# Optimization experiments

Hardware: AMD Instinct MI355X
Metric: run time of the kernel (lower is better)

Reference implementation:

```python
import jax, jax.numpy as jnp
import numpy as np

B = 64          # batches
T = 65536       # total packed tokens
X = 512         # token feature dim
K = 5           # io pairs
Y = X * K       # extra dim = 2560
H = 512         # hidden


def setup_inputs() -> dict:
    key = jax.random.key(0)
    ks = jax.random.split(key, 13)
    s = 0.02  # weight scale
    return {
        "ps_data": jax.random.normal(ks[0], (T, X), jnp.float32),
        "io_embed": jax.random.normal(ks[1], (B, K, X), jnp.float32),
        "segment_ids": jnp.sort(jax.random.randint(ks[2], (T,), 0, B, dtype=jnp.int32)),
        # attention_fc: Linear(X+Y,512) -> ReLU -> Linear(512,512) -> ReLU -> Linear(512,1)
        "W1": jax.random.normal(ks[3], (X + Y, H), jnp.float32) * s,
        "b1": jnp.zeros((H,), jnp.float32),
        "W2": jax.random.normal(ks[4], (H, H), jnp.float32) * s,
        "b2": jnp.zeros((H,), jnp.float32),
        "W3": jax.random.normal(ks[5], (H, 1), jnp.float32) * s,
        "b3": jnp.zeros((1,), jnp.float32),
        # final_fc: Linear(512,512) -> ReLU -> Linear(512,2)
        "Wf1": jax.random.normal(ks[6], (H, H), jnp.float32) * s,
        "bf1": jnp.zeros((H,), jnp.float32),
        "Wf2": jax.random.normal(ks[7], (H, 2), jnp.float32) * s,
        "bf2": jnp.zeros((2,), jnp.float32),
    }


def reference(ps_data, io_embed, segment_ids, W1, b1, W2, b2, W3, b3, Wf1, bf1, Wf2, bf2):
    # io_embed (B,K,X) -> (B,Y); gather per token by its batch index
    extra = io_embed.reshape(B, -1)[segment_ids]            # (T, Y)
    h = jnp.concatenate([ps_data, extra], axis=1)           # (T, X+Y)
    h = jax.nn.relu(h @ W1 + b1)
    h = jax.nn.relu(h @ W2 + b2)
    logits = (h @ W3 + b3)[:, 0]                            # (T,)
    # per-segment softmax over ragged segments
    m = jax.lax.stop_gradient(
        jax.ops.segment_max(logits, segment_ids, num_segments=B))
    e = jnp.exp(logits - m[segment_ids])
    denom = jax.ops.segment_sum(e, segment_ids, num_segments=B)
    w = e / denom[segment_ids]                              # (T,)
    pooled = jax.ops.segment_sum(w[:, None] * ps_data, segment_ids,
                                 num_segments=B)            # (B, X)
    # final_fc
    return jax.nn.relu(pooled @ Wf1 + bf1) @ Wf2 + bf2      # (B, 2)
```

## Files before the change

### kernel.cpp

```cpp
#include <hip/hip_runtime.h>

#define T_TOK 65536
#define BATCH 64
#define XDIM  512
#define HDIM  512
#define YDIM  2560

#define BK 64
#define GM_TM 256
#define GM_TN 128

#define SB_KC 64
#define SB_KS 40
#define SB_BG 8

#define PREP_CONV   16384
#define PREP_TRANS  2048
#define PREP_SB     320

typedef float  f32x16 __attribute__((ext_vector_type(16)));
typedef __bf16 bf16x8 __attribute__((ext_vector_type(8)));

__device__ __forceinline__ unsigned short f2bf(float f) {
    unsigned int u = __float_as_uint(f);
    return (unsigned short)((u + 0x7FFFu + ((u >> 16) & 1u)) >> 16);
}

__device__ __forceinline__ float bf2f(unsigned short u) {
    return __uint_as_float((unsigned int)u << 16);
}

__device__ __forceinline__ void load_lds16(const unsigned short* g, unsigned short* l) {
    __builtin_amdgcn_global_load_lds(
        (const __attribute__((address_space(1))) unsigned int*)g,
        (__attribute__((address_space(3))) unsigned int*)l, 16, 0, 0);
}

__device__ __forceinline__ int lower_bound_seg(const int* __restrict__ s, int n, int v) {
    int lo = 0, hi = n;
    while (lo < hi) { int mid = (lo + hi) >> 1; if (s[mid] < v) lo = mid + 1; else hi = mid; }
    return lo;
}

__global__ __launch_bounds__(256) void prep_kernel(const float* __restrict__ ps,
                                                   unsigned short* __restrict__ psb,
                                                   const float* __restrict__ W1,
                                                   const float* __restrict__ W2,
                                                   unsigned short* __restrict__ w1t,
                                                   unsigned short* __restrict__ w2t,
                                                   const float* __restrict__ io,
                                                   float* __restrict__ partial) {
    __shared__ float sio[SB_BG][SB_KC];
    const int blk = blockIdx.x;
    const int t = threadIdx.x;

    if (blk < PREP_CONV) {
        size_t idx = (size_t)blk * 256 + t;
        const float4* s4 = reinterpret_cast<const float4*>(ps) + idx * 2;
        float4 a = s4[0], b = s4[1];
        ushort4 o0, o1;
        o0.x = f2bf(a.x); o0.y = f2bf(a.y); o0.z = f2bf(a.z); o0.w = f2bf(a.w);
        o1.x = f2bf(b.x); o1.y = f2bf(b.y); o1.z = f2bf(b.z); o1.w = f2bf(b.w);
        reinterpret_cast<ushort4*>(psb)[idx * 2 + 0] = o0;
        reinterpret_cast<ushort4*>(psb)[idx * 2 + 1] = o1;
    } else if (blk < PREP_CONV + PREP_TRANS) {
        int bb = blk - PREP_CONV;
        const float* src = bb < 1024 ? W1 : W2;
        unsigned short* dst = bb < 1024 ? w1t : w2t;
        int idx = (bb & 1023) * 256 + t;
        int nn = idx >> 9, kk = idx & 511;
        dst[idx] = f2bf(src[(size_t)kk * 512 + nn]);
    } else {
        int sb = blk - PREP_CONV - PREP_TRANS;
        int s = sb >> 3, g = sb & 7;
        for (int i = t; i < SB_BG * SB_KC; i += 256) {
            int bb = i >> 6, kk = i & 63;
            sio[bb][kk] = io[(size_t)(g * SB_BG + bb) * YDIM + s * SB_KC + kk];
        }
        __syncthreads();
        float acc[SB_BG][2] = {};
        const int k0 = 512 + s * SB_KC;
        #pragma unroll 4
        for (int kk = 0; kk < SB_KC; kk++) {
            float wa = W1[(size_t)(k0 + kk) * 512 + t];
            float wb = W1[(size_t)(k0 + kk) * 512 + t + 256];
            #pragma unroll
            for (int bb = 0; bb < SB_BG; bb++) {
                acc[bb][0] += sio[bb][kk] * wa;
                acc[bb][1] += sio[bb][kk] * wb;
            }
        }
        #pragma unroll
        for (int bb = 0; bb < SB_BG; bb++) {
            int b = g * SB_BG + bb;
            partial[((size_t)s * BATCH + b) * 512 + t]       = acc[bb][0];
            partial[((size_t)s * BATCH + b) * 512 + t + 256] = acc[bb][1];
        }
    }
}

__global__ __launch_bounds__(256) void segbias_reduce(const float* __restrict__ partial,
                                                      float* __restrict__ segbias) {
    int idx = blockIdx.x * 256 + threadIdx.x;
    float s = 0.f;
    #pragma unroll
    for (int i = 0; i < SB_KS; i++) s += partial[(size_t)i * BATCH * 512 + idx];
    segbias[idx] = s;
}

#define FRAG_AT(sh, R, c) (*reinterpret_cast<const bf16x8*>(&(sh)[((R) * 8 + (((c) ^ ((R) & 7)))) * 8]))

__global__ __launch_bounds__(512) void gemm1_kernel(const unsigned short* __restrict__ psb,
                                                    const unsigned short* __restrict__ w1t,
                                                    const float* __restrict__ segbias,
                                                    const float* __restrict__ b1,
                                                    const int* __restrict__ segids,
                                                    unsigned short* __restrict__ h1) {
    __shared__ unsigned short shA[GM_TM * BK];
    __shared__ unsigned short shB[GM_TN * BK];

    const int bid = blockIdx.x;
    const int xcd = bid & 7;
    const int j = bid >> 3;
    const int n0 = (j & 3) * GM_TN;
    const int m0 = ((j >> 2) * 8 + xcd) * GM_TM;
    const int t = threadIdx.x;
    const int w = t >> 6, L = t & 63;
    const int mbase = (w >> 1) * 64, nbase = (w & 1) * 64;
    const int l31 = L & 31, lh = L >> 5;

    f32x16 acc[2][2] = {};

    for (int kt = 0; kt < XDIM; kt += BK) {
        #pragma unroll
        for (int i_ = 0; i_ < 4; i_++) {
            int g_ = i_ * 512 + t;
            int r_ = g_ >> 3, c_ = g_ & 7, cs_ = c_ ^ (r_ & 7);
            load_lds16(psb + (size_t)(m0 + r_) * XDIM + kt + cs_ * 8, &shA[g_ * 8]);
        }
        #pragma unroll
        for (int i_ = 0; i_ < 2; i_++) {
            int g_ = i_ * 512 + t;
            int r_ = g_ >> 3, c_ = g_ & 7, cs_ = c_ ^ (r_ & 7);
            load_lds16(w1t + (size_t)(n0 + r_) * HDIM + kt + cs_ * 8, &shB[g_ * 8]);
        }
        __syncthreads();
        #pragma unroll
        for (int ks = 0; ks < 4; ks++) {
            const int c = ks * 2 + lh;
            bf16x8 af[2], bfr[2];
            #pragma unroll
            for (int i = 0; i < 2; i++)  af[i]  = FRAG_AT(shA, mbase + i * 32 + l31, c);
            #pragma unroll
            for (int jj = 0; jj < 2; jj++) bfr[jj] = FRAG_AT(shB, nbase + jj * 32 + l31, c);
            #pragma unroll
            for (int i = 0; i < 2; i++)
                #pragma unroll
                for (int jj = 0; jj < 2; jj++)
                    acc[i][jj] = __builtin_amdgcn_mfma_f32_32x32x16_bf16(af[i], bfr[jj], acc[i][jj], 0, 0, 0);
        }
        __syncthreads();
    }

    float b1v[2];
    #pragma unroll
    for (int jj = 0; jj < 2; jj++) b1v[jj] = b1[n0 + nbase + jj * 32 + l31];
    #pragma unroll
    for (int i = 0; i < 2; i++) {
        #pragma unroll
        for (int r = 0; r < 16; r++) {
            int gm = m0 + mbase + i * 32 + (r & 3) + 8 * (r >> 2) + 4 * lh;
            int sg = segids[gm];
            const float* sb = segbias + (size_t)sg * HDIM;
            #pragma unroll
            for (int jj = 0; jj < 2; jj++) {
                int gn = n0 + nbase + jj * 32 + l31;
                float v = acc[i][jj][r] + sb[gn] + b1v[jj];
                v = v > 0.f ? v : 0.f;
                h1[(size_t)gm * HDIM + gn] = f2bf(v);
            }
        }
    }
}

__global__ __launch_bounds__(512) void gemm2_kernel(const unsigned short* __restrict__ h1,
                                                    const unsigned short* __restrict__ w2t,
                                                    const float* __restrict__ b2,
                                                    const float* __restrict__ w3,
                                                    float* __restrict__ logits8) {
    __shared__ unsigned short shA[GM_TM * BK];
    __shared__ unsigned short shB[GM_TN * BK];

    const int bid = blockIdx.x;
    const int xcd = bid & 7;
    const int j = bid >> 3;
    const int n0 = (j & 3) * GM_TN;
    const int m0 = ((j >> 2) * 8 + xcd) * GM_TM;
    const int t = threadIdx.x;
    const int w = t >> 6, L = t & 63;
    const int mbase = (w >> 1) * 64, nbase = (w & 1) * 64;
    const int l31 = L & 31, lh = L >> 5;

    f32x16 acc[2][2] = {};

    for (int kt = 0; kt < HDIM; kt += BK) {
        #pragma unroll
        for (int i_ = 0; i_ < 4; i_++) {
            int g_ = i_ * 512 + t;
            int r_ = g_ >> 3, c_ = g_ & 7, cs_ = c_ ^ (r_ & 7);
            load_lds16(h1 + (size_t)(m0 + r_) * HDIM + kt + cs_ * 8, &shA[g_ * 8]);
        }
        #pragma unroll
        for (int i_ = 0; i_ < 2; i_++) {
            int g_ = i_ * 512 + t;
            int r_ = g_ >> 3, c_ = g_ & 7, cs_ = c_ ^ (r_ & 7);
            load_lds16(w2t + (size_t)(n0 + r_) * HDIM + kt + cs_ * 8, &shB[g_ * 8]);
        }
        __syncthreads();
        #pragma unroll
        for (int ks = 0; ks < 4; ks++) {
            const int c = ks * 2 + lh;
            bf16x8 af[2], bfr[2];
            #pragma unroll
            for (int i = 0; i < 2; i++)  af[i]  = FRAG_AT(shA, mbase + i * 32 + l31, c);
            #pragma unroll
            for (int jj = 0; jj < 2; jj++) bfr[jj] = FRAG_AT(shB, nbase + jj * 32 + l31, c);
            #pragma unroll
            for (int i = 0; i < 2; i++)
                #pragma unroll
                for (int jj = 0; jj < 2; jj++)
                    acc[i][jj] = __builtin_amdgcn_mfma_f32_32x32x16_bf16(af[i], bfr[jj], acc[i][jj], 0, 0, 0);
        }
        __syncthreads();
    }

    float w3v[2], b2v[2];
    #pragma unroll
    for (int jj = 0; jj < 2; jj++) {
        int gn = n0 + nbase + jj * 32 + l31;
        w3v[jj] = w3[gn];
        b2v[jj] = b2[gn];
    }
    const int slice = (j & 3) * 2 + (w & 1);
    #pragma unroll
    for (int i = 0; i < 2; i++) {
        #pragma unroll
        for (int r = 0; r < 16; r++) {
            float p = 0.f;
            #pragma unroll
            for (int jj = 0; jj < 2; jj++) {
                float h2 = acc[i][jj][r] + b2v[jj];
                h2 = h2 > 0.f ? h2 : 0.f;
                p += h2 * w3v[jj];
            }
            p += __shfl_xor(p, 1, 64);
            p += __shfl_xor(p, 2, 64);
            p += __shfl_xor(p, 4, 64);
            p += __shfl_xor(p, 8, 64);
            p += __shfl_xor(p, 16, 64);
            if (l31 == 0)
                logits8[(size_t)slice * T_TOK + m0 + mbase + i * 32 +
                        (r & 3) + 8 * (r >> 2) + 4 * lh] = p;
        }
    }
}

__global__ __launch_bounds__(512) void pool_kernel(const unsigned short* __restrict__ psb,
                                                   const float* __restrict__ logits8,
                                                   const int* __restrict__ segids,
                                                   float* __restrict__ pooled16) {
    const int s = blockIdx.x;
    const int b = blockIdx.y;
    const int t = threadIdx.x;
    __shared__ float wv[512];
    __shared__ float sred[8];
    const int start = lower_bound_seg(segids, T_TOK, b);
    const int end   = lower_bound_seg(segids, T_TOK, b + 1);

    float m = -3.4e38f;
    for (int i = start + t; i < end; i += 512) {
        float l = 0.f;
        #pragma unroll
        for (int k = 0; k < 8; k++) l += logits8[(size_t)k * T_TOK + i];
        m = fmaxf(m, l);
    }
    for (int d = 32; d; d >>= 1) m = fmaxf(m, __shfl_down(m, d, 64));
    if ((t & 63) == 0) sred[t >> 6] = m;
    __syncthreads();
    m = sred[0];
    #pragma unroll
    for (int k = 1; k < 8; k++) m = fmaxf(m, sred[k]);
    __syncthreads();
    float ss = 0.f;
    for (int i = start + t; i < end; i += 512) {
        float l = 0.f;
        #pragma unroll
        for (int k = 0; k < 8; k++) l += logits8[(size_t)k * T_TOK + i];
        ss += __expf(l - m);
    }
    for (int d = 32; d; d >>= 1) ss += __shfl_down(ss, d, 64);
    if ((t & 63) == 0) sred[t >> 6] = ss;
    __syncthreads();
    float denom = 0.f;
    #pragma unroll
    for (int k = 0; k < 8; k++) denom += sred[k];
    const float inv = 1.f / denom;

    const int n = end - start;
    const int per = (n + 15) >> 4;
    const int s0 = start + s * per;
    const int s1 = min(s0 + per, end);
    float acc = 0.f;
    for (int base = s0; base < s1; base += 512) {
        int cnt = min(512, s1 - base);
        __syncthreads();
        if (t < cnt) {
            float l = 0.f;
            #pragma unroll
            for (int k = 0; k < 8; k++) l += logits8[(size_t)k * T_TOK + base + t];
            wv[t] = __expf(l - m) * inv;
        }
        __syncthreads();
        for (int i = 0; i < cnt; i++)
            acc += wv[i] * bf2f(psb[(size_t)(base + i) * XDIM + t]);
    }
    pooled16[((size_t)s * BATCH + b) * XDIM + t] = acc;
}

__global__ __launch_bounds__(512) void final_kernel(const float* __restrict__ pooled16,
                                                    const float* __restrict__ wf1,
                                                    const float* __restrict__ bf1,
                                                    const float* __restrict__ wf2,
                                                    const float* __restrict__ bf2,
                                                    float* __restrict__ out) {
    const int b = blockIdx.x;
    const int t = threadIdx.x;
    __shared__ float sp[512];
    __shared__ float r0s[8], r1s[8];
    float pv = 0.f;
    #pragma unroll
    for (int k = 0; k < 16; k++) pv += pooled16[((size_t)k * BATCH + b) * XDIM + t];
    sp[t] = pv;
    __syncthreads();
    float acc = bf1[t];
    #pragma unroll 4
    for (int k = 0; k < 512; k++) acc += sp[k] * wf1[(size_t)k * 512 + t];
    float h = fmaxf(acc, 0.f);
    float p0 = h * wf2[t * 2 + 0];
    float p1 = h * wf2[t * 2 + 1];
    for (int d = 32; d; d >>= 1) { p0 += __shfl_down(p0, d, 64); p1 += __shfl_down(p1, d, 64); }
    if ((t & 63) == 0) { r0s[t >> 6] = p0; r1s[t >> 6] = p1; }
    __syncthreads();
    if (t == 0) {
        float a = 0.f, c = 0.f;
        #pragma unroll
        for (int i = 0; i < 8; i++) { a += r0s[i]; c += r1s[i]; }
        out[b * 2 + 0] = a + bf2[0];
        out[b * 2 + 1] = c + bf2[1];
    }
}

extern "C" void kernel_launch(void* const* d_in, const int* in_sizes, int n_in,
                              void* d_out, int out_size, void* d_ws, size_t ws_size,
                              hipStream_t stream) {
    const float* ps  = (const float*)d_in[0];
    const float* io  = (const float*)d_in[1];
    const int*   seg = (const int*)d_in[2];
    const float* W1  = (const float*)d_in[3];
    const float* b1  = (const float*)d_in[4];
    const float* W2  = (const float*)d_in[5];
    const float* b2  = (const float*)d_in[6];
    const float* W3  = (const float*)d_in[7];
    const float* Wf1 = (const float*)d_in[9];
    const float* bf1 = (const float*)d_in[10];
    const float* Wf2 = (const float*)d_in[11];
    const float* bf2 = (const float*)d_in[12];
    float* out = (float*)d_out;

    char* ws = (char*)d_ws;
    float*          segbias  = (float*)(ws + 0);
    unsigned short* w1t      = (unsigned short*)(ws + 131072);
    unsigned short* w2t      = (unsigned short*)(ws + 655360);
    float*          logits8  = (float*)(ws + 1179648);
    float*          pooled16 = (float*)(ws + 3276800);
    float*          partial  = (float*)(ws + 5373952);
    unsigned short* psb      = (unsigned short*)(ws + 16777216);
    unsigned short* h1       = (unsigned short*)(ws + 83886080);

    prep_kernel<<<PREP_CONV + PREP_TRANS + PREP_SB, 256, 0, stream>>>(
        ps, psb, W1, W2, w1t, w2t, io, partial);
    segbias_reduce<<<128, 256, 0, stream>>>(partial, segbias);
    gemm1_kernel<<<(T_TOK / GM_TM) * 4, 512, 0, stream>>>(psb, w1t, segbias, b1, seg, h1);
    gemm2_kernel<<<(T_TOK / GM_TM) * 4, 512, 0, stream>>>(h1, w2t, b2, W3, logits8);
    pool_kernel<<<dim3(16, 64), 512, 0, stream>>>(psb, logits8, seg, pooled16);
    final_kernel<<<64, 512, 0, stream>>>(pooled16, Wf1, bf1, Wf2, bf2, out);
}
```

Measured before the change: 398.4 us.

## Fuse fp32-to-bf16 conversion of tokens into gemm1 and use 16x16x32 MFMA

Removes the standalone conversion pass that wrote a bf16 copy of ps_data; gemm1 now loads fp32 rows, truncates them to bf16 in registers and stores them swizzled into LDS, while the pooling kernel reads fp32 directly. Both GEMMs switch from 32x32x16 to 16x16x32 bf16 MFMA tiles with a 4x4 accumulator grid per wave. This saves the conversion kernel's write and re-read of the bf16 buffer, but gemm1 re-reads fp32 A for each of the 4 N tiles, loses the async direct-to-LDS loads for A, and truncation replaces round-to-nearest.

```diff
diff --git a/kernel.cpp b/kernel.cpp
--- a/kernel.cpp
+++ b/kernel.cpp
@@ -14,11 +14,10 @@
 #define SB_KS 40
 #define SB_BG 8
 
-#define PREP_CONV   16384
 #define PREP_TRANS  2048
 #define PREP_SB     320
 
-typedef float  f32x16 __attribute__((ext_vector_type(16)));
+typedef float  f32x4  __attribute__((ext_vector_type(4)));
 typedef __bf16 bf16x8 __attribute__((ext_vector_type(8)));
 
 __device__ __forceinline__ unsigned short f2bf(float f) {
@@ -26,8 +25,8 @@
     return (unsigned short)((u + 0x7FFFu + ((u >> 16) & 1u)) >> 16);
 }
 
-__device__ __forceinline__ float bf2f(unsigned short u) {
-    return __uint_as_float((unsigned int)u << 16);
+__device__ __forceinline__ unsigned int pack_bf2(float hi, float lo) {
+    return (__float_as_uint(hi) & 0xffff0000u) | (__float_as_uint(lo) >> 16);
 }
 
 __device__ __forceinline__ void load_lds16(const unsigned short* g, unsigned short* l) {
@@ -42,9 +41,7 @@
     return lo;
 }
 
-__global__ __launch_bounds__(256) void prep_kernel(const float* __restrict__ ps,
-                                                   unsigned short* __restrict__ psb,
-                                                   const float* __restrict__ W1,
+__global__ __launch_bounds__(256) void prep_kernel(const float* __restrict__ W1,
                                                    const float* __restrict__ W2,
                                                    unsigned short* __restrict__ w1t,
                                                    unsigned short* __restrict__ w2t,
@@ -54,24 +51,15 @@
     const int blk = blockIdx.x;
     const int t = threadIdx.x;
 
-    if (blk < PREP_CONV) {
-        size_t idx = (size_t)blk * 256 + t;
-        const float4* s4 = reinterpret_cast<const float4*>(ps) + idx * 2;
-        float4 a = s4[0], b = s4[1];
-        ushort4 o0, o1;
-        o0.x = f2bf(a.x); o0.y = f2bf(a.y); o0.z = f2bf(a.z); o0.w = f2bf(a.w);
-        o1.x = f2bf(b.x); o1.y = f2bf(b.y); o1.z = f2bf(b.z); o1.w = f2bf(b.w);
-        reinterpret_cast<ushort4*>(psb)[idx * 2 + 0] = o0;
-        reinterpret_cast<ushort4*>(psb)[idx * 2 + 1] = o1;
-    } else if (blk < PREP_CONV + PREP_TRANS) {
-        int bb = blk - PREP_CONV;
+    if (blk < PREP_TRANS) {
+        int bb = blk;
         const float* src = bb < 1024 ? W1 : W2;
         unsigned short* dst = bb < 1024 ? w1t : w2t;
         int idx = (bb & 1023) * 256 + t;
         int nn = idx >> 9, kk = idx & 511;
         dst[idx] = f2bf(src[(size_t)kk * 512 + nn]);
     } else {
-        int sb = blk - PREP_CONV - PREP_TRANS;
+        int sb = blk - PREP_TRANS;
         int s = sb >> 3, g = sb & 7;
         for (int i = t; i < SB_BG * SB_KC; i += 256) {
             int bb = i >> 6, kk = i & 63;
@@ -110,7 +98,7 @@
 
 #define FRAG_AT(sh, R, c) (*reinterpret_cast<const bf16x8*>(&(sh)[((R) * 8 + (((c) ^ ((R) & 7)))) * 8]))
 
-__global__ __launch_bounds__(512) void gemm1_kernel(const unsigned short* __restrict__ psb,
+__global__ __launch_bounds__(512) void gemm1_kernel(const float* __restrict__ ps,
                                                     const unsigned short* __restrict__ w1t,
                                                     const float* __restrict__ segbias,
                                                     const float* __restrict__ b1,
@@ -127,55 +115,60 @@
     const int t = threadIdx.x;
     const int w = t >> 6, L = t & 63;
     const int mbase = (w >> 1) * 64, nbase = (w & 1) * 64;
-    const int l31 = L & 31, lh = L >> 5;
-
-    f32x16 acc[2][2] = {};
+    const int lrow = L & 15, lq = L >> 4;
+
+    f32x4 acc[4][4] = {};
 
     for (int kt = 0; kt < XDIM; kt += BK) {
-        #pragma unroll
-        for (int i_ = 0; i_ < 4; i_++) {
-            int g_ = i_ * 512 + t;
-            int r_ = g_ >> 3, c_ = g_ & 7, cs_ = c_ ^ (r_ & 7);
-            load_lds16(psb + (size_t)(m0 + r_) * XDIM + kt + cs_ * 8, &shA[g_ * 8]);
-        }
         #pragma unroll
         for (int i_ = 0; i_ < 2; i_++) {
             int g_ = i_ * 512 + t;
             int r_ = g_ >> 3, c_ = g_ & 7, cs_ = c_ ^ (r_ & 7);
             load_lds16(w1t + (size_t)(n0 + r_) * HDIM + kt + cs_ * 8, &shB[g_ * 8]);
         }
-        __syncthreads();
-        #pragma unroll
-        for (int ks = 0; ks < 4; ks++) {
-            const int c = ks * 2 + lh;
-            bf16x8 af[2], bfr[2];
-            #pragma unroll
-            for (int i = 0; i < 2; i++)  af[i]  = FRAG_AT(shA, mbase + i * 32 + l31, c);
-            #pragma unroll
-            for (int jj = 0; jj < 2; jj++) bfr[jj] = FRAG_AT(shB, nbase + jj * 32 + l31, c);
-            #pragma unroll
-            for (int i = 0; i < 2; i++)
+        #pragma unroll
+        for (int i_ = 0; i_ < 4; i_++) {
+            int g_ = i_ * 512 + t;
+            int r_ = g_ >> 3, c_ = g_ & 7;
+            const float4* s4 = reinterpret_cast<const float4*>(
+                ps + (size_t)(m0 + r_) * XDIM + kt + c_ * 8);
+            float4 x = s4[0], y = s4[1];
+            uint4 pk;
+            pk.x = pack_bf2(x.y, x.x);
+            pk.y = pack_bf2(x.w, x.z);
+            pk.z = pack_bf2(y.y, y.x);
+            pk.w = pack_bf2(y.w, y.z);
+            int cs_ = c_ ^ (r_ & 7);
+            *reinterpret_cast<uint4*>(&shA[(r_ * 8 + cs_) * 8]) = pk;
+        }
+        __syncthreads();
+        #pragma unroll
+        for (int ks = 0; ks < BK; ks += 32) {
+            bf16x8 af[4], bfr[4];
+            #pragma unroll
+            for (int i = 0; i < 4; i++) af[i] = FRAG_AT(shA, mbase + i * 16 + lrow, (ks >> 3) + lq);
+            #pragma unroll
+            for (int jj = 0; jj < 4; jj++) bfr[jj] = FRAG_AT(shB, nbase + jj * 16 + lrow, (ks >> 3) + lq);
+            #pragma unroll
+            for (int i = 0; i < 4; i++)
                 #pragma unroll
-                for (int jj = 0; jj < 2; jj++)
-                    acc[i][jj] = __builtin_amdgcn_mfma_f32_32x32x16_bf16(af[i], bfr[jj], acc[i][jj], 0, 0, 0);
-        }
-        __syncthreads();
-    }
-
-    float b1v[2];
-    #pragma unroll
-    for (int jj = 0; jj < 2; jj++) b1v[jj] = b1[n0 + nbase + jj * 32 + l31];
-    #pragma unroll
-    for (int i = 0; i < 2; i++) {
-        #pragma unroll
-        for (int r = 0; r < 16; r++) {
-            int gm = m0 + mbase + i * 32 + (r & 3) + 8 * (r >> 2) + 4 * lh;
+                for (int jj = 0; jj < 4; jj++)
+                    acc[i][jj] = __builtin_amdgcn_mfma_f32_16x16x32_bf16(af[i], bfr[jj], acc[i][jj], 0, 0, 0);
+        }
+        __syncthreads();
+    }
+
+    #pragma unroll
+    for (int i = 0; i < 4; i++) {
+        #pragma unroll
+        for (int r = 0; r < 4; r++) {
+            int gm = m0 + mbase + i * 16 + lq * 4 + r;
             int sg = segids[gm];
             const float* sb = segbias + (size_t)sg * HDIM;
             #pragma unroll
-            for (int jj = 0; jj < 2; jj++) {
-                int gn = n0 + nbase + jj * 32 + l31;
-                float v = acc[i][jj][r] + sb[gn] + b1v[jj];
+            for (int jj = 0; jj < 4; jj++) {
+                int gn = n0 + nbase + jj * 16 + lrow;
+                float v = acc[i][jj][r] + sb[gn] + b1[gn];
                 v = v > 0.f ? v : 0.f;
                 h1[(size_t)gm * HDIM + gn] = f2bf(v);
             }
@@ -199,9 +192,9 @@
     const int t = threadIdx.x;
     const int w = t >> 6, L = t & 63;
     const int mbase = (w >> 1) * 64, nbase = (w & 1) * 64;
-    const int l31 = L & 31, lh = L >> 5;
-
-    f32x16 acc[2][2] = {};
+    const int lrow = L & 15, lq = L >> 4;
+
+    f32x4 acc[4][4] = {};
 
     for (int kt = 0; kt < HDIM; kt += BK) {
         #pragma unroll
@@ -218,37 +211,36 @@
         }
         __syncthreads();
         #pragma unroll
-        for (int ks = 0; ks < 4; ks++) {
-            const int c = ks * 2 + lh;
-            bf16x8 af[2], bfr[2];
-            #pragma unroll
-            for (int i = 0; i < 2; i++)  af[i]  = FRAG_AT(shA, mbase + i * 32 + l31, c);
-            #pragma unroll
-            for (int jj = 0; jj < 2; jj++) bfr[jj] = FRAG_AT(shB, nbase + jj * 32 + l31, c);
-            #pragma unroll
-            for (int i = 0; i < 2; i++)
+        for (int ks = 0; ks < BK; ks += 32) {
+            bf16x8 af[4], bfr[4];
+            #pragma unroll
+            for (int i = 0; i < 4; i++) af[i] = FRAG_AT(shA, mbase + i * 16 + lrow, (ks >> 3) + lq);
+            #pragma unroll
+            for (int jj = 0; jj < 4; jj++) bfr[jj] = FRAG_AT(shB, nbase + jj * 16 + lrow, (ks >> 3) + lq);
+            #pragma unroll
+            for (int i = 0; i < 4; i++)
                 #pragma unroll
-                for (int jj = 0; jj < 2; jj++)
-                    acc[i][jj] = __builtin_amdgcn_mfma_f32_32x32x16_bf16(af[i], bfr[jj], acc[i][jj], 0, 0, 0);
-        }
-        __syncthreads();
-    }
-
-    float w3v[2], b2v[2];
-    #pragma unroll
-    for (int jj = 0; jj < 2; jj++) {
-        int gn = n0 + nbase + jj * 32 + l31;
+                for (int jj = 0; jj < 4; jj++)
+                    acc[i][jj] = __builtin_amdgcn_mfma_f32_16x16x32_bf16(af[i], bfr[jj], acc[i][jj], 0, 0, 0);
+        }
+        __syncthreads();
+    }
+
+    float w3v[4], b2v[4];
+    #pragma unroll
+    for (int jj = 0; jj < 4; jj++) {
+        int gn = n0 + nbase + jj * 16 + lrow;
         w3v[jj] = w3[gn];
         b2v[jj] = b2[gn];
     }
     const int slice = (j & 3) * 2 + (w & 1);
     #pragma unroll
-    for (int i = 0; i < 2; i++) {
-        #pragma unroll
-        for (int r = 0; r < 16; r++) {
+    for (int i = 0; i < 4; i++) {
+        #pragma unroll
+        for (int r = 0; r < 4; r++) {
             float p = 0.f;
             #pragma unroll
-            for (int jj = 0; jj < 2; jj++) {
+            for (int jj = 0; jj < 4; jj++) {
                 float h2 = acc[i][jj][r] + b2v[jj];
                 h2 = h2 > 0.f ? h2 : 0.f;
                 p += h2 * w3v[jj];
@@ -257,15 +249,13 @@
             p += __shfl_xor(p, 2, 64);
             p += __shfl_xor(p, 4, 64);
             p += __shfl_xor(p, 8, 64);
-            p += __shfl_xor(p, 16, 64);
-            if (l31 == 0)
-                logits8[(size_t)slice * T_TOK + m0 + mbase + i * 32 +
-                        (r & 3) + 8 * (r >> 2) + 4 * lh] = p;
-        }
-    }
-}
-
-__global__ __launch_bounds__(512) void pool_kernel(const unsigned short* __restrict__ psb,
+            if (lrow == 0)
+                logits8[(size_t)slice * T_TOK + m0 + mbase + i * 16 + lq * 4 + r] = p;
+        }
+    }
+}
+
+__global__ __launch_bounds__(512) void pool_kernel(const float* __restrict__ ps,
                                                    const float* __restrict__ logits8,
                                                    const int* __restrict__ segids,
                                                    float* __restrict__ pooled16) {
@@ -322,7 +312,7 @@
         }
         __syncthreads();
         for (int i = 0; i < cnt; i++)
-            acc += wv[i] * bf2f(psb[(size_t)(base + i) * XDIM + t]);
+            acc += wv[i] * ps[(size_t)(base + i) * XDIM + t];
     }
     pooled16[((size_t)s * BATCH + b) * XDIM + t] = acc;
 }
@@ -384,14 +374,12 @@
     float*          logits8  = (float*)(ws + 1179648);
     float*          pooled16 = (float*)(ws + 3276800);
     float*          partial  = (float*)(ws + 5373952);
-    unsigned short* psb      = (unsigned short*)(ws + 16777216);
-    unsigned short* h1       = (unsigned short*)(ws + 83886080);
-
-    prep_kernel<<<PREP_CONV + PREP_TRANS + PREP_SB, 256, 0, stream>>>(
-        ps, psb, W1, W2, w1t, w2t, io, partial);
+    unsigned short* h1       = (unsigned short*)(ws + 16777216);
+
+    prep_kernel<<<PREP_TRANS + PREP_SB, 256, 0, stream>>>(W1, W2, w1t, w2t, io, partial);
     segbias_reduce<<<128, 256, 0, stream>>>(partial, segbias);
-    gemm1_kernel<<<(T_TOK / GM_TM) * 4, 512, 0, stream>>>(psb, w1t, segbias, b1, seg, h1);
+    gemm1_kernel<<<(T_TOK / GM_TM) * 4, 512, 0, stream>>>(ps, w1t, segbias, b1, seg, h1);
     gemm2_kernel<<<(T_TOK / GM_TM) * 4, 512, 0, stream>>>(h1, w2t, b2, W3, logits8);
-    pool_kernel<<<dim3(16, 64), 512, 0, stream>>>(psb, logits8, seg, pooled16);
+    pool_kernel<<<dim3(16, 64), 512, 0, stream>>>(ps, logits8, seg, pooled16);
     final_kernel<<<64, 512, 0, stream>>>(pooled16, Wf1, bf1, Wf2, bf2, out);
 }
```

Result: no change. 391.9 us (-1.6%).
